# Kernel tuning notes

Hardware: AMD Instinct MI355X
Metric: run time of the kernel (lower is better)

Reference implementation:

```python
import jax, jax.numpy as jnp
import numpy as np

D_MODEL, D_K, D_V, H = 1024, 64, 64, 16
B, N = 4, 2048


def setup_inputs() -> dict:
    key = jax.random.key(0)
    ks = jax.random.split(key, 11)
    s = 0.02
    return {
        "Q": jax.random.normal(ks[0], (B, N, D_MODEL), jnp.float32),
        "K": jax.random.normal(ks[1], (B, N, D_MODEL), jnp.float32),
        "V": jax.random.normal(ks[2], (B, N, D_MODEL), jnp.float32),
        # stacked per-head projection weights: [h, d_model, d_k]
        "Wq": jax.random.normal(ks[3], (H, D_MODEL, D_K), jnp.float32) * s,
        "bq": jax.random.normal(ks[4], (H, D_K), jnp.float32) * s,
        "Wk": jax.random.normal(ks[5], (H, D_MODEL, D_K), jnp.float32) * s,
        "bk": jax.random.normal(ks[6], (H, D_K), jnp.float32) * s,
        "Wv": jax.random.normal(ks[7], (H, D_MODEL, D_V), jnp.float32) * s,
        "bv": jax.random.normal(ks[8], (H, D_V), jnp.float32) * s,
        "Wo": jax.random.normal(ks[9], (H * D_V, D_MODEL), jnp.float32) * s,
        "bo": jax.random.normal(ks[10], (D_MODEL,), jnp.float32) * s,
        "apply_mask": 1,
    }


def reference(Q, K, V, Wq, bq, Wk, bk, Wv, bv, Wo, bo, apply_mask):
    # fused per-head projections: [b, h, n, d_k]
    q = jnp.einsum("bnd,hdk->bhnk", Q, Wq) + bq[None, :, None, :]
    k = jnp.einsum("bnd,hdk->bhnk", K, Wk) + bk[None, :, None, :]
    v = jnp.einsum("bnd,hdv->bhnv", V, Wv) + bv[None, :, None, :]
    scores = jnp.einsum("bhnk,bhmk->bhnm", q, k) / jnp.sqrt(
        jnp.asarray(D_K, q.dtype)
    )
    if apply_mask:
        n = Q.shape[1]
        causal = jnp.tril(jnp.ones((n, n), dtype=bool))
        scores = jnp.where(causal[None, None], scores, -jnp.inf)
    weights = jax.nn.softmax(scores, axis=-1)
    out = jnp.einsum("bhnm,bhmv->bhnv", weights, v)
    # concat heads: [b, n, h*d_v]
    out = out.transpose(0, 2, 1, 3).reshape(Q.shape[0], Q.shape[1], H * D_V)
    return out @ Wo + bo
```

## Files before the change

### kernel.cpp

```cpp
#include <hip/hip_runtime.h>
#include <hip/hip_bf16.h>

#define H 16
#define DM 1024
#define DK 64
#define B_ 4
#define N_ 2048

typedef __attribute__((ext_vector_type(8))) short bf16x8;
typedef __attribute__((ext_vector_type(4))) short s16x4;
typedef __attribute__((ext_vector_type(2))) unsigned int u32x2;
typedef __attribute__((ext_vector_type(4))) float f32x4;

static __device__ __forceinline__ short f2bs(float x) {
    __hip_bfloat16 b = __float2bfloat16(x);
    return *reinterpret_cast<short*>(&b);
}

static __device__ __forceinline__ void async16(const void* g, void* l) {
    __builtin_amdgcn_global_load_lds(
        (const __attribute__((address_space(1))) void*)g,
        (__attribute__((address_space(3))) void*)l, 16, 0, 0);
}

static __device__ __forceinline__ unsigned packbf(float lo, float hi) {
    return __builtin_amdgcn_perm(__float_as_uint(hi), __float_as_uint(lo), 0x07060302u);
}

__global__ __launch_bounds__(256) void prep_kernel(
    const float* __restrict__ Q, const float* __restrict__ K, const float* __restrict__ V,
    const float* __restrict__ Wq, const float* __restrict__ Wk,
    const float* __restrict__ Wv, const float* __restrict__ Wo,
    short* __restrict__ Qb, short* __restrict__ Kb, short* __restrict__ Vb,
    short* __restrict__ wqT, short* __restrict__ wkT,
    short* __restrict__ wvT, short* __restrict__ woT)
{
    int y = blockIdx.y;
    if (y < 3) {
        const float* s = (y == 0) ? Q : (y == 1) ? K : V;
        short* d = (y == 0) ? Qb : (y == 1) ? Kb : Vb;
        size_t i = ((size_t)blockIdx.x * 256 + threadIdx.x) * 8;
        f32x4 a = *(const f32x4*)(s + i);
        f32x4 b = *(const f32x4*)(s + i + 4);
        bf16x8 p;
        #pragma unroll
        for (int j = 0; j < 4; ++j) { p[j] = f2bs(a[j]); p[4 + j] = f2bs(b[j]); }
        *(bf16x8*)(d + i) = p;
        return;
    }
    if (blockIdx.x >= 1024) return;
    __shared__ float tile[64][65];
    int z = blockIdx.x >> 8;
    int bx = blockIdx.x & 255;
    int t = threadIdx.x;
    int tj = t & 63, ti = t >> 6;

    if (z < 3) {
        const float* src = (z == 0) ? Wq : (z == 1) ? Wk : Wv;
        short* dst = (z == 0) ? wqT : (z == 1) ? wkT : wvT;
        int h = bx >> 4;
        int dmt = bx & 15;
        #pragma unroll
        for (int r = 0; r < 16; ++r) {
            int i = r * 4 + ti;
            tile[i][tj] = src[((size_t)h * 1024 + dmt * 64 + i) * 64 + tj];
        }
        __syncthreads();
        #pragma unroll
        for (int r = 0; r < 16; ++r) {
            int dk = r * 4 + ti;
            dst[((size_t)h * 64 + dk) * 1024 + dmt * 64 + tj] = f2bs(tile[tj][dk]);
        }
    } else {
        int kt = bx >> 4;
        int nt = bx & 15;
        #pragma unroll
        for (int r = 0; r < 16; ++r) {
            int i = r * 4 + ti;
            tile[i][tj] = Wo[((size_t)kt * 64 + i) * 1024 + nt * 64 + tj];
        }
        __syncthreads();
        #pragma unroll
        for (int r = 0; r < 16; ++r) {
            int jn = r * 4 + ti;
            woT[((size_t)nt * 64 + jn) * 1024 + kt * 64 + tj] = f2bs(tile[tj][jn]);
        }
    }
}

static __device__ __forceinline__ void gemm_mainloop(
    const short* __restrict__ A, const short* __restrict__ BT,
    int rowM0, int colN0, char* As, char* Bs, f32x4 (&acc)[4][4])
{
    int tid = threadIdx.x;
    int lane = tid & 63, w = tid >> 6;
    int l16 = lane & 15, quad = lane >> 4;
    int wm = w >> 1, wn = w & 1;
    int xg = (quad ^ ((l16 >> 1) & 3)) << 4;

    int r0 = w * 32 + (lane >> 2);
    int gsl = ((lane & 3) ^ ((lane >> 3) & 3)) << 4;
    int dst0 = w * 2048 + lane * 16;
    const char* Ag0 = (const char*)A + (size_t)(rowM0 + r0) * 2048 + gsl;
    const char* Ag1 = (const char*)A + (size_t)(rowM0 + r0 + 16) * 2048 + gsl;
    const char* Bg0 = (const char*)BT + (size_t)(colN0 + r0) * 2048 + gsl;
    const char* Bg1 = (const char*)BT + (size_t)(colN0 + r0 + 16) * 2048 + gsl;

    char* la0 = As + dst0;
    char* la1 = As + dst0 + 1024;
    char* lb0 = Bs + dst0;
    char* lb1 = Bs + dst0 + 1024;

    for (int it = 0; it < 32; ++it) {
        size_t kb = (size_t)it * 64;
        if (it) __syncthreads();
        async16(Ag0 + kb, la0);
        async16(Ag1 + kb, la1);
        async16(Bg0 + kb, lb0);
        async16(Bg1 + kb, lb1);
        __syncthreads();

        bf16x8 a[4], b[4];
        #pragma unroll
        for (int i = 0; i < 4; ++i)
            a[i] = *(const bf16x8*)(As + (wm * 64 + i * 16 + l16) * 64 + xg);
        #pragma unroll
        for (int j = 0; j < 4; ++j)
            b[j] = *(const bf16x8*)(Bs + (wn * 64 + j * 16 + l16) * 64 + xg);
        #pragma unroll
        for (int i = 0; i < 4; ++i)
            #pragma unroll
            for (int j = 0; j < 4; ++j)
                acc[i][j] = __builtin_amdgcn_mfma_f32_16x16x32_bf16(a[i], b[j], acc[i][j], 0, 0, 0);
    }
}

__global__ __launch_bounds__(256) void proj_gemm(
    const short* __restrict__ Qb, const short* __restrict__ Kb, const short* __restrict__ Vb,
    const short* __restrict__ wqT, const short* __restrict__ wkT, const short* __restrict__ wvT,
    const float* __restrict__ bq, const float* __restrict__ bk, const float* __restrict__ bv,
    short* __restrict__ qbuf, short* __restrict__ kbuf, short* __restrict__ vTbuf)
{
    __shared__ char As[8192], Bs[8192];
    int which = blockIdx.z;
    const short* A  = (which == 0) ? Qb : (which == 1) ? Kb : Vb;
    const short* BT = (which == 0) ? wqT : (which == 1) ? wkT : wvT;
    const float* bias = (which == 0) ? bq : (which == 1) ? bk : bv;

    int rowM0 = blockIdx.x * 128;
    int colN0 = blockIdx.y * 128;

    f32x4 acc[4][4];
    #pragma unroll
    for (int i = 0; i < 4; ++i)
        #pragma unroll
        for (int j = 0; j < 4; ++j) acc[i][j] = (f32x4){0.f, 0.f, 0.f, 0.f};

    gemm_mainloop(A, BT, rowM0, colN0, As, Bs, acc);

    int lane = threadIdx.x & 63, w = threadIdx.x >> 6;
    int l16 = lane & 15, quad = lane >> 4;
    int wm = w >> 1, wn = w & 1;

    if (which == 2) {
        #pragma unroll
        for (int j = 0; j < 4; ++j) {
            int col = colN0 + wn * 64 + j * 16 + l16;
            int hh = col >> 6, dv = col & 63;
            float bs = bias[col];
            #pragma unroll
            for (int i = 0; i < 4; ++i) {
                int rowb = rowM0 + wm * 64 + i * 16 + quad * 4;
                int bb = rowb >> 11, n0 = rowb & 2047;
                s16x4 pk;
                #pragma unroll
                for (int r = 0; r < 4; ++r) pk[r] = f2bs(acc[i][j][r] + bs);
                *(s16x4*)(vTbuf + (((size_t)bb * H + hh) * DK + dv) * N_ + n0) = pk;
            }
        }
    } else {
        short* dst = (which == 0) ? qbuf : kbuf;
        float scl = (which == 0) ? 0.180336880f : 1.0f;
        #pragma unroll
        for (int j = 0; j < 4; ++j) {
            int col = colN0 + wn * 64 + j * 16 + l16;
            float bs = bias[col];
            #pragma unroll
            for (int i = 0; i < 4; ++i) {
                int rowb = rowM0 + wm * 64 + i * 16 + quad * 4;
                #pragma unroll
                for (int r = 0; r < 4; ++r)
                    dst[(size_t)(rowb + r) * 1024 + col] = f2bs((acc[i][j][r] + bs) * scl);
            }
        }
    }
}

__global__ __launch_bounds__(256) void out_gemm(
    const short* __restrict__ obuf, const short* __restrict__ woT,
    const float* __restrict__ bo, float* __restrict__ out)
{
    __shared__ char As[8192], Bs[8192];
    int rowM0 = blockIdx.x * 128;
    int colN0 = blockIdx.y * 128;

    f32x4 acc[4][4];
    #pragma unroll
    for (int i = 0; i < 4; ++i)
        #pragma unroll
        for (int j = 0; j < 4; ++j) acc[i][j] = (f32x4){0.f, 0.f, 0.f, 0.f};

    gemm_mainloop(obuf, woT, rowM0, colN0, As, Bs, acc);

    int lane = threadIdx.x & 63, w = threadIdx.x >> 6;
    int l16 = lane & 15, quad = lane >> 4;
    int wm = w >> 1, wn = w & 1;

    #pragma unroll
    for (int j = 0; j < 4; ++j) {
        int col = colN0 + wn * 64 + j * 16 + l16;
        float bs = bo[col];
        #pragma unroll
        for (int i = 0; i < 4; ++i) {
            int rowb = rowM0 + wm * 64 + i * 16 + quad * 4;
            #pragma unroll
            for (int r = 0; r < 4; ++r)
                out[(size_t)(rowb + r) * 1024 + col] = acc[i][j][r] + bs;
        }
    }
}

__global__ __launch_bounds__(256) void flash_kernel(
    const short* __restrict__ qbuf, const short* __restrict__ kbuf, const short* __restrict__ vT,
    short* __restrict__ obuf, const int* __restrict__ amask)
{
    __shared__ short Ks[2][4096];
    __shared__ short Vs[2][4096];
    __shared__ char  plds[4][2048];

    int bid = blockIdx.x;
    int g = bid & 7, idx = bid >> 3;
    int bh = g * 8 + (idx >> 4);
    int xq = idx & 15;
    int b = bh >> 4, h = bh & 15;

    int tid = threadIdx.x;
    int lane = tid & 63, wave = tid >> 6;
    int l16 = lane & 15, quad = lane >> 4;
    int msk = amask[0];

    int i8 = lane >> 3, i7 = lane & 7;
    int sg = (i7 ^ i8) << 4;
    int pk0 = i8 * 4 + wave;
    int skey = wave * 16 + i8;
    int ldst = wave * 2048 + lane * 16;

    const char* kbase = (const char*)(kbuf + (size_t)b * 2048 * 1024 + h * 64);
    const char* vbase = (const char*)(vT + ((size_t)(b * 16 + h) * 64) * 2048);

    int m7 = l16 & 7;
    int g0 = (quad ^ m7) << 4;
    int g1 = ((4 | quad) ^ m7) << 4;

    char* pw = plds[wave];
    int prd0 = l16 * 128 + g0;
    int prd1 = l16 * 128 + g1;
    int pwa[4];
    #pragma unroll
    for (int r = 0; r < 4; ++r) {
        int row = quad * 4 + r;
        pwa[r] = row * 128 + (((l16 >> 1) ^ (row & 7)) << 4) + ((l16 & 1) << 3);
    }

    for (int pass = 0; pass < 2; ++pass) {
        int qt = pass ? (31 - xq) : xq;
        int qw = qt * 64 + wave * 16;
        int nkb = msk ? (qt + 1) : 32;

        const short* qp = qbuf + ((size_t)(b * 2048 + qw + l16)) * 1024 + h * 64;
        bf16x8 aq0 = *(const bf16x8*)(qp + quad * 8);
        bf16x8 aq1 = *(const bf16x8*)(qp + 32 + quad * 8);

        f32x4 o[4];
        float lsum[4];
        #pragma unroll
        for (int i = 0; i < 4; ++i) { o[i] = (f32x4){0.f, 0.f, 0.f, 0.f}; lsum[i] = 0.f; }

        async16(kbase + (size_t)pk0 * 2048 + sg, (char*)Ks[0] + ldst);
        async16(kbase + (size_t)(pk0 + 32) * 2048 + sg, (char*)Ks[0] + ldst + 1024);
        async16(vbase + (size_t)skey * 4096 + sg, (char*)Vs[0] + ldst);
        async16(vbase + (size_t)(skey + 8) * 4096 + sg, (char*)Vs[0] + ldst + 1024);

        for (int ib = 0; ib < nkb; ++ib) {
            __syncthreads();
            int cur = ib & 1;
            if (ib + 1 < nkb) {
                int nb = (ib + 1) & 1;
                size_t kb2 = (size_t)(ib + 1) * 64;
                async16(kbase + (kb2 + pk0) * 2048 + sg, (char*)Ks[nb] + ldst);
                async16(kbase + (kb2 + pk0 + 32) * 2048 + sg, (char*)Ks[nb] + ldst + 1024);
                async16(vbase + (size_t)skey * 4096 + kb2 * 2 + sg, (char*)Vs[nb] + ldst);
                async16(vbase + (size_t)(skey + 8) * 4096 + kb2 * 2 + sg, (char*)Vs[nb] + ldst + 1024);
            }
            int kb = ib * 64;

            f32x4 s[4];
            __builtin_amdgcn_s_setprio(1);
            #pragma unroll
            for (int nt = 0; nt < 4; ++nt) {
                const char* kr = (const char*)Ks[cur] + (nt * 16 + l16) * 128;
                bf16x8 b0 = *(const bf16x8*)(kr + g0);
                bf16x8 b1 = *(const bf16x8*)(kr + g1);
                f32x4 t = (f32x4){0.f, 0.f, 0.f, 0.f};
                t = __builtin_amdgcn_mfma_f32_16x16x32_bf16(aq0, b0, t, 0, 0, 0);
                t = __builtin_amdgcn_mfma_f32_16x16x32_bf16(aq1, b1, t, 0, 0, 0);
                s[nt] = t;
            }
            __builtin_amdgcn_s_setprio(0);

            if (msk && (kb + 63 > qw)) {
                #pragma unroll
                for (int r = 0; r < 4; ++r) {
                    int row = qw + quad * 4 + r;
                    #pragma unroll
                    for (int nt = 0; nt < 4; ++nt) {
                        int col = kb + l16 * 4 + nt;
                        if (col > row) s[nt][r] = -3e38f;
                    }
                }
            }

            __builtin_amdgcn_wave_barrier();
            #pragma unroll
            for (int r = 0; r < 4; ++r) {
                float p0 = __builtin_amdgcn_exp2f(s[0][r]);
                float p1 = __builtin_amdgcn_exp2f(s[1][r]);
                float p2 = __builtin_amdgcn_exp2f(s[2][r]);
                float p3 = __builtin_amdgcn_exp2f(s[3][r]);
                lsum[r] += (p0 + p1) + (p2 + p3);
                u32x2 pk;
                pk[0] = packbf(p0, p1);
                pk[1] = packbf(p2, p3);
                *(u32x2*)(pw + pwa[r]) = pk;
            }
            __builtin_amdgcn_wave_barrier();
            bf16x8 ap0 = *(const bf16x8*)(pw + prd0);
            bf16x8 ap1 = *(const bf16x8*)(pw + prd1);
            __builtin_amdgcn_wave_barrier();

            __builtin_amdgcn_s_setprio(1);
            #pragma unroll
            for (int vb = 0; vb < 4; ++vb) {
                const char* vr = (const char*)Vs[cur] + (vb * 16 + l16) * 128;
                bf16x8 v0 = *(const bf16x8*)(vr + g0);
                bf16x8 v1 = *(const bf16x8*)(vr + g1);
                o[vb] = __builtin_amdgcn_mfma_f32_16x16x32_bf16(ap0, v0, o[vb], 0, 0, 0);
                o[vb] = __builtin_amdgcn_mfma_f32_16x16x32_bf16(ap1, v1, o[vb], 0, 0, 0);
            }
            __builtin_amdgcn_s_setprio(0);
        }

        #pragma unroll
        for (int r = 0; r < 4; ++r) {
            float t = lsum[r];
            #pragma unroll
            for (int off = 1; off < 16; off <<= 1) t += __shfl_xor(t, off, 64);
            float inv = 1.0f / t;
            int row = qw + quad * 4 + r;
            #pragma unroll
            for (int vb = 0; vb < 4; ++vb)
                obuf[((size_t)(b * 2048 + row)) * 1024 + h * 64 + vb * 16 + l16] =
                    f2bs(o[vb][r] * inv);
        }
        __syncthreads();
    }
}

extern "C" void kernel_launch(void* const* d_in, const int* in_sizes, int n_in,
                              void* d_out, int out_size, void* d_ws, size_t ws_size,
                              hipStream_t stream)
{
    const float* Q  = (const float*)d_in[0];
    const float* K  = (const float*)d_in[1];
    const float* V  = (const float*)d_in[2];
    const float* Wq = (const float*)d_in[3];
    const float* bq = (const float*)d_in[4];
    const float* Wk = (const float*)d_in[5];
    const float* bk = (const float*)d_in[6];
    const float* Wv = (const float*)d_in[7];
    const float* bv = (const float*)d_in[8];
    const float* Wo = (const float*)d_in[9];
    const float* bo = (const float*)d_in[10];
    const int* amask = (const int*)d_in[11];
    float* out = (float*)d_out;

    char* ws = (char*)d_ws;
    const size_t SZ = (size_t)B_ * N_ * DM * sizeof(short);
    const size_t SZW = (size_t)H * DK * DM * sizeof(short);
    short* Qb    = (short*)ws; ws += SZ;
    short* Kb    = (short*)ws; ws += SZ;
    short* Vb    = (short*)ws; ws += SZ;
    short* qbuf  = (short*)ws; ws += SZ;
    short* kbuf  = (short*)ws; ws += SZ;
    short* vTbuf = (short*)ws; ws += SZ;
    short* wqT   = (short*)ws; ws += SZW;
    short* wkT   = (short*)ws; ws += SZW;
    short* wvT   = (short*)ws; ws += SZW;
    short* woT   = (short*)ws; ws += SZW;
    short* obuf  = Qb;

    prep_kernel<<<dim3(4096, 4), dim3(256), 0, stream>>>(Q, K, V, Wq, Wk, Wv, Wo,
                                                         Qb, Kb, Vb, wqT, wkT, wvT, woT);
    proj_gemm<<<dim3(64, 8, 3), dim3(256), 0, stream>>>(Qb, Kb, Vb, wqT, wkT, wvT,
                                                        bq, bk, bv, qbuf, kbuf, vTbuf);
    flash_kernel<<<dim3(1024), dim3(256), 0, stream>>>(qbuf, kbuf, vTbuf, obuf, amask);
    out_gemm<<<dim3(64, 8), dim3(256), 0, stream>>>(obuf, woT, bo, out);
}
```

Baseline: 323.9 us.

## Triple-buffer GEMM mainloop with async LDS prefetch three stages ahead

Replaces the single-buffered load-then-compute GEMM mainloop with a 3-stage ring of LDS buffers. The loads for k-step it+3 are issued asynchronously while step it computes, with vmcnt waits and barriers in place of full syncthreads. The goal is to hide global memory latency behind MFMA work in the projection and output GEMMs. The cost is tripled LDS per block (48 KB), which can reduce occupancy, plus hand-managed waitcnt logic.

```diff
diff --git a/kernel.cpp b/kernel.cpp
--- a/kernel.cpp
+++ b/kernel.cpp
@@ -90,7 +90,7 @@
 
 static __device__ __forceinline__ void gemm_mainloop(
     const short* __restrict__ A, const short* __restrict__ BT,
-    int rowM0, int colN0, char* As, char* Bs, f32x4 (&acc)[4][4])
+    int rowM0, int colN0, char* lds, f32x4 (&acc)[4][4])
 {
     int tid = threadIdx.x;
     int lane = tid & 63, w = tid >> 6;
@@ -102,24 +102,32 @@
     int gsl = ((lane & 3) ^ ((lane >> 3) & 3)) << 4;
     int dst0 = w * 2048 + lane * 16;
     const char* Ag0 = (const char*)A + (size_t)(rowM0 + r0) * 2048 + gsl;
-    const char* Ag1 = (const char*)A + (size_t)(rowM0 + r0 + 16) * 2048 + gsl;
+    const char* Ag1 = Ag0 + 16 * 2048;
     const char* Bg0 = (const char*)BT + (size_t)(colN0 + r0) * 2048 + gsl;
-    const char* Bg1 = (const char*)BT + (size_t)(colN0 + r0 + 16) * 2048 + gsl;
-
-    char* la0 = As + dst0;
-    char* la1 = As + dst0 + 1024;
-    char* lb0 = Bs + dst0;
-    char* lb1 = Bs + dst0 + 1024;
-
+    const char* Bg1 = Bg0 + 16 * 2048;
+
+    #pragma unroll
+    for (int t = 0; t < 3; ++t) {
+        size_t kb = (size_t)t * 64;
+        char* As = lds + t * 16384;
+        char* Bs = As + 8192;
+        async16(Ag0 + kb, As + dst0);
+        async16(Ag1 + kb, As + dst0 + 1024);
+        async16(Bg0 + kb, Bs + dst0);
+        async16(Bg1 + kb, Bs + dst0 + 1024);
+    }
+
+    int c0 = 0;
     for (int it = 0; it < 32; ++it) {
-        size_t kb = (size_t)it * 64;
-        if (it) __syncthreads();
-        async16(Ag0 + kb, la0);
-        async16(Ag1 + kb, la1);
-        async16(Bg0 + kb, lb0);
-        async16(Bg1 + kb, lb1);
-        __syncthreads();
-
+        if (it < 30)       asm volatile("s_waitcnt vmcnt(8)" ::: "memory");
+        else if (it == 30) asm volatile("s_waitcnt vmcnt(4)" ::: "memory");
+        else               asm volatile("s_waitcnt vmcnt(0)" ::: "memory");
+        __builtin_amdgcn_s_barrier();
+        asm volatile("" ::: "memory");
+        __builtin_amdgcn_sched_barrier(0);
+
+        const char* As = lds + c0;
+        const char* Bs = As + 8192;
         bf16x8 a[4], b[4];
         #pragma unroll
         for (int i = 0; i < 4; ++i)
@@ -132,6 +140,21 @@
             #pragma unroll
             for (int j = 0; j < 4; ++j)
                 acc[i][j] = __builtin_amdgcn_mfma_f32_16x16x32_bf16(a[i], b[j], acc[i][j], 0, 0, 0);
+
+        asm volatile("" ::: "memory");
+        __builtin_amdgcn_s_barrier();
+        __builtin_amdgcn_sched_barrier(0);
+        if (it + 3 < 32) {
+            size_t kb = (size_t)(it + 3) * 64;
+            char* Aw = lds + c0;
+            char* Bw = Aw + 8192;
+            async16(Ag0 + kb, Aw + dst0);
+            async16(Ag1 + kb, Aw + dst0 + 1024);
+            async16(Bg0 + kb, Bw + dst0);
+            async16(Bg1 + kb, Bw + dst0 + 1024);
+        }
+        c0 += 16384;
+        if (c0 == 49152) c0 = 0;
     }
 }
 
@@ -141,7 +164,7 @@
     const float* __restrict__ bq, const float* __restrict__ bk, const float* __restrict__ bv,
     short* __restrict__ qbuf, short* __restrict__ kbuf, short* __restrict__ vTbuf)
 {
-    __shared__ char As[8192], Bs[8192];
+    __shared__ char lds[49152];
     int which = blockIdx.z;
     const short* A  = (which == 0) ? Qb : (which == 1) ? Kb : Vb;
     const short* BT = (which == 0) ? wqT : (which == 1) ? wkT : wvT;
@@ -156,7 +179,7 @@
         #pragma unroll
         for (int j = 0; j < 4; ++j) acc[i][j] = (f32x4){0.f, 0.f, 0.f, 0.f};
 
-    gemm_mainloop(A, BT, rowM0, colN0, As, Bs, acc);
+    gemm_mainloop(A, BT, rowM0, colN0, lds, acc);
 
     int lane = threadIdx.x & 63, w = threadIdx.x >> 6;
     int l16 = lane & 15, quad = lane >> 4;
@@ -200,7 +223,7 @@
     const short* __restrict__ obuf, const short* __restrict__ woT,
     const float* __restrict__ bo, float* __restrict__ out)
 {
-    __shared__ char As[8192], Bs[8192];
+    __shared__ char lds[49152];
     int rowM0 = blockIdx.x * 128;
     int colN0 = blockIdx.y * 128;
 
@@ -210,7 +233,7 @@
         #pragma unroll
         for (int j = 0; j < 4; ++j) acc[i][j] = (f32x4){0.f, 0.f, 0.f, 0.f};
 
-    gemm_mainloop(obuf, woT, rowM0, colN0, As, Bs, acc);
+    gemm_mainloop(obuf, woT, rowM0, colN0, lds, acc);
 
     int lane = threadIdx.x & 63, w = threadIdx.x >> 6;
     int l16 = lane & 15, quad = lane >> 4;
```

After: 310.3 us. 4.2% less time.
